# Kernel tuning notes

Hardware: AMD Instinct MI355X
Metric: run time of the kernel (lower is better)

## Reference

```python
import jax, jax.numpy as jnp
import numpy as np

B, T, F, H, L = 16384, 24, 7, 8, 4
DENSE = [T * H, 1024, 2048, 4]


def setup_inputs() -> dict:
    key = jax.random.key(0)
    d = {"x": jax.random.normal(jax.random.fold_in(key, 0), (B, T, F), jnp.float32)}
    k = 1
    s = 1.0 / np.sqrt(H)  # torch LSTM init bound
    for l in range(L):
        in_dim = F if l == 0 else H
        for name, shape in [("Wih", (4 * H, in_dim)), ("Whh", (4 * H, H)), ("bih", (4 * H,)), ("bhh", (4 * H,))]:
            d[f"{name}{l}"] = jax.random.uniform(jax.random.fold_in(key, k), shape, jnp.float32, -s, s)
            k += 1
    for i in range(1, len(DENSE)):
        si = 1.0 / np.sqrt(DENSE[i - 1])
        d[f"Wd{i}"] = jax.random.uniform(jax.random.fold_in(key, k), (DENSE[i], DENSE[i - 1]), jnp.float32, -si, si)
        k += 1
        d[f"bd{i}"] = jax.random.uniform(jax.random.fold_in(key, k), (DENSE[i],), jnp.float32, -si, si)
        k += 1
    return d


def _lstm_layer(xs, Wih, Whh, b):
    # xs: [T, B, in] -> ys: [T, B, H]; torch gate order i,f,g,o
    Hn = Whh.shape[1]
    h0 = jnp.zeros((xs.shape[1], Hn), xs.dtype)

    def step(carry, xt):
        h, c = carry
        z = xt @ Wih.T + h @ Whh.T + b  # [B, 4H]
        i, f, g, o = jnp.split(z, 4, axis=-1)
        c = jax.nn.sigmoid(f) * c + jax.nn.sigmoid(i) * jnp.tanh(g)
        h = jax.nn.sigmoid(o) * jnp.tanh(c)
        return (h, c), h

    (_, _), ys = jax.lax.scan(step, (h0, h0), xs)
    return ys


def _forward(x, lstm_params, dense_params):
    xs = jnp.transpose(x, (1, 0, 2))  # [T, B, F]
    for (Wih, Whh, bih, bhh) in lstm_params:
        xs = _lstm_layer(xs, Wih, Whh, bih + bhh)
    out = jnp.transpose(xs, (1, 0, 2)).reshape(x.shape[0], T * H)  # [B, 192]
    (W1, b1), (W2, b2), (W3, b3) = dense_params
    out = jax.nn.relu(out @ W1.T + b1)
    out = jax.nn.relu(out @ W2.T + b2)
    return out @ W3.T + b3  # [B, num_classes]


def reference(x, Wih0, Whh0, bih0, bhh0, Wih1, Whh1, bih1, bhh1, Wih2, Whh2, bih2, bhh2, Wih3, Whh3, bih3, bhh3, Wd1, bd1, Wd2, bd2, Wd3, bd3):
    lstm_params = [(Wih0, Whh0, bih0, bhh0), (Wih1, Whh1, bih1, bhh1), (Wih2, Whh2, bih2, bhh2), (Wih3, Whh3, bih3, bhh3)]
    dense_params = [(Wd1, bd1), (Wd2, bd2), (Wd3, bd3)]
    return _forward(x, lstm_params, dense_params)
```

## Files before the change

### kernel.cpp

```cpp
#include <hip/hip_runtime.h>
#include <hip/hip_bf16.h>

typedef __attribute__((ext_vector_type(4))) float f32x4;
typedef __attribute__((ext_vector_type(16))) float f32x16;
typedef __attribute__((ext_vector_type(2))) float f32x2;
typedef __attribute__((ext_vector_type(8))) short bf16x8;

__device__ __forceinline__ ushort f2bf(float f) {
    union { float f; uint u; } v; v.f = f;
    uint u = v.u;
    return (ushort)((u + 0x7fffu + ((u >> 16) & 1u)) >> 16);
}
__device__ __forceinline__ float sigm(float x) {
    return __builtin_amdgcn_rcpf(1.0f + __builtin_amdgcn_exp2f(x * -1.442695040888963f));
}
__device__ __forceinline__ float tanh_(float x) {
    return 2.0f * __builtin_amdgcn_rcpf(1.0f + __builtin_amdgcn_exp2f(x * -2.885390081777927f)) - 1.0f;
}

typedef const __attribute__((address_space(1))) unsigned int ga_u32;
typedef __attribute__((address_space(3))) unsigned int lds_u32;
__device__ __forceinline__ void g2l16(const void* g, void* l) {
    __builtin_amdgcn_global_load_lds((ga_u32*)(unsigned long long)g,
                                     (lds_u32*)(unsigned int)(unsigned long long)l,
                                     16, 0, 0);
}

struct LstmW {
    const float* wih[4];
    const float* whh[4];
    const float* bih[4];
    const float* bhh[4];
};

__device__ __forceinline__ void gates8p(const f32x2 w01[8], const f32x2 w23[8],
                                        const float xv8[8], f32x2& a01, f32x2& a23) {
#pragma unroll
    for (int k = 0; k < 8; ++k) {
        f32x2 xv = {xv8[k], xv8[k]};
        a01 += w01[k] * xv;
        a23 += w23[k] * xv;
    }
}
__device__ __forceinline__ void cellup(f32x2 a01, f32x2 a23, float& h, float& c) {
    c = sigm(a01.y) * c + sigm(a01.x) * tanh_(a23.x);
    h = sigm(a23.y) * tanh_(c);
}
__device__ __forceinline__ void ld8(const float* p, float v[8]) {
    float4 a = *(const float4*)p;
    float4 b = *(const float4*)(p + 4);
    v[0] = a.x; v[1] = a.y; v[2] = a.z; v[3] = a.w;
    v[4] = b.x; v[5] = b.y; v[6] = b.z; v[7] = b.w;
}

__global__ __launch_bounds__(256) void pre_kernel(const float* __restrict__ x, LstmW p,
                                                  ushort* __restrict__ Y,
                                                  const float* __restrict__ W1,
                                                  const float* __restrict__ W2,
                                                  ushort* __restrict__ W1b,
                                                  ushort* __restrict__ W2b,
                                                  const float* __restrict__ b3,
                                                  float* __restrict__ out) {
    __shared__ float xs[32 * 168];
    __shared__ float hb[32 * 200];

    const int tid = threadIdx.x;
    if (blockIdx.x >= 512) {
        const int tg = (blockIdx.x - 512) * 256 + tid;
        if (tg < 16384) {
            float4 bv = {b3[0], b3[1], b3[2], b3[3]};
            ((float4*)out)[tg] = bv;
        }
#pragma unroll
        for (int s = 0; s < 4; ++s) {
            int i = tg + s * 143360;
            const float4* src; ushort4* dst; int off;
            if (i < 49152) { src = (const float4*)W1; dst = (ushort4*)W1b; off = i; }
            else { src = (const float4*)W2; dst = (ushort4*)W2b; off = i - 49152; }
            float4 v = src[off];
            ushort4 r; r.x = f2bf(v.x); r.y = f2bf(v.y); r.z = f2bf(v.z); r.w = f2bf(v.w);
            dst[off] = r;
        }
        return;
    }

    const int e0 = blockIdx.x * 32;
    {
        const float4* s = (const float4*)(x + (size_t)e0 * 168);
        float4* d = (float4*)xs;
        for (int i = tid; i < 1344; i += 256) d[i] = s[i];
    }
    __syncthreads();

    const int el = tid >> 3, j = tid & 7;
    float* hr = hb + el * 200;
    const float* xr = xs + el * 168;

    f32x2 wx01[8], wx23[8], wh01[8], wh23[8], b01, b23;

    {
        const float* Wih = p.wih[0];
        const float* Whh = p.whh[0];
#pragma unroll
        for (int k = 0; k < 7; ++k) {
            wx01[k] = {Wih[(0 + j) * 7 + k], Wih[(8 + j) * 7 + k]};
            wx23[k] = {Wih[(16 + j) * 7 + k], Wih[(24 + j) * 7 + k]};
        }
#pragma unroll
        for (int k = 0; k < 8; ++k) {
            wh01[k] = {Whh[(0 + j) * 8 + k], Whh[(8 + j) * 8 + k]};
            wh23[k] = {Whh[(16 + j) * 8 + k], Whh[(24 + j) * 8 + k]};
        }
        b01 = {p.bih[0][j] + p.bhh[0][j], p.bih[0][8 + j] + p.bhh[0][8 + j]};
        b23 = {p.bih[0][16 + j] + p.bhh[0][16 + j], p.bih[0][24 + j] + p.bhh[0][24 + j]};

        float h = 0.f, c = 0.f;
        {
            f32x2 a01 = b01, a23 = b23;
#pragma unroll
            for (int k = 0; k < 7; ++k) {
                f32x2 xv = {xr[k], xr[k]};
                a01 += wx01[k] * xv; a23 += wx23[k] * xv;
            }
            cellup(a01, a23, h, c);
            hr[j] = h;
        }
        for (int t = 1; t < 24; ++t) {
            f32x2 a01 = b01, a23 = b23;
#pragma unroll
            for (int k = 0; k < 7; ++k) {
                f32x2 xv = {xr[t * 7 + k], xr[t * 7 + k]};
                a01 += wx01[k] * xv; a23 += wx23[k] * xv;
            }
            float hp[8]; ld8(&hr[(t - 1) * 8], hp);
            gates8p(wh01, wh23, hp, a01, a23);
            cellup(a01, a23, h, c);
            hr[t * 8 + j] = h;
        }
    }

#pragma unroll
    for (int l = 1; l < 4; ++l) {
        const float* Wih = p.wih[l];
        const float* Whh = p.whh[l];
#pragma unroll
        for (int k = 0; k < 8; ++k) {
            wx01[k] = {Wih[(0 + j) * 8 + k], Wih[(8 + j) * 8 + k]};
            wx23[k] = {Wih[(16 + j) * 8 + k], Wih[(24 + j) * 8 + k]};
            wh01[k] = {Whh[(0 + j) * 8 + k], Whh[(8 + j) * 8 + k]};
            wh23[k] = {Whh[(16 + j) * 8 + k], Whh[(24 + j) * 8 + k]};
        }
        b01 = {p.bih[l][j] + p.bhh[l][j], p.bih[l][8 + j] + p.bhh[l][8 + j]};
        b23 = {p.bih[l][16 + j] + p.bhh[l][16 + j], p.bih[l][24 + j] + p.bhh[l][24 + j]};

        float h = 0.f, c = 0.f;
        {
            float xin[8]; ld8(&hr[0], xin);
            f32x2 a01 = b01, a23 = b23;
            gates8p(wx01, wx23, xin, a01, a23);
            cellup(a01, a23, h, c);
            hr[j] = h;
            if (l == 3) Y[((size_t)(e0 + el) * 24) * 8 + j] = f2bf(h);
        }
        for (int t = 1; t < 24; ++t) {
            float xin[8]; ld8(&hr[t * 8], xin);
            float hp[8];  ld8(&hr[(t - 1) * 8], hp);
            f32x2 a01 = b01, a23 = b23;
            gates8p(wx01, wx23, xin, a01, a23);
            gates8p(wh01, wh23, hp, a01, a23);
            cellup(a01, a23, h, c);
            hr[t * 8 + j] = h;
            if (l == 3) Y[((size_t)(e0 + el) * 24 + t) * 8 + j] = f2bf(h);
        }
    }
}

template <int KDIM, bool FUSE3>
__device__ __forceinline__ void gemm_body(const ushort* __restrict__ A,
                                          const ushort* __restrict__ W,
                                          const float* __restrict__ bias,
                                          ushort* __restrict__ Hout,
                                          const float* __restrict__ W3,
                                          float* __restrict__ outf, int N) {
    constexpr int SMEMN = FUSE3 ? 16896 : 16384;
    __shared__ alignas(16) ushort smem[SMEMN];
    __shared__ alignas(16) float w3s[FUSE3 ? 528 : 1];
    ushort* As = smem;
    ushort* Ws = smem + 8192;

    const int tid = threadIdx.x;
    const int m0 = blockIdx.x * 128;
    const int n0 = blockIdx.y * 128;
    const int lane = tid & 63;
    const int wv = tid >> 6;
    const int wm = (wv & 1) * 64;
    const int wn = (wv >> 1) * 64;
    const int l31 = lane & 31;
    const int kh = lane >> 5;

    if (FUSE3) {
        for (int i = tid; i < 512; i += 256)
            w3s[(i >> 7) * 132 + (i & 127)] = W3[(size_t)(i >> 7) * 2048 + n0 + (i & 127)];
    }

    const int lrow = lane >> 3;
    const int lchunk = (lane & 7) ^ lrow;
    const ushort* Ag = A + (size_t)(m0 + wv * 32 + lrow) * KDIM + lchunk * 8;
    const ushort* Wg = W + (size_t)(n0 + wv * 32 + lrow) * KDIM + lchunk * 8;
    ushort* Ald = As + wv * 2048;
    ushort* Wld = Ws + wv * 2048;

    const int r7 = l31 & 7;
    const int arow0 = (wm + l31) * 64;
    const int brow0 = (wn + l31) * 64;

    f32x16 acc[2][2];
#pragma unroll
    for (int mi = 0; mi < 2; ++mi)
#pragma unroll
        for (int ni = 0; ni < 2; ++ni)
#pragma unroll
            for (int r = 0; r < 16; ++r) acc[mi][ni][r] = 0.f;

    for (int k0 = 0; k0 < KDIM; k0 += 64) {
#pragma unroll
        for (int c = 0; c < 4; ++c)
            g2l16(Ag + (size_t)c * 8 * KDIM + k0, Ald + c * 512);
#pragma unroll
        for (int c = 0; c < 4; ++c)
            g2l16(Wg + (size_t)c * 8 * KDIM + k0, Wld + c * 512);
        __syncthreads();

#pragma unroll
        for (int ks = 0; ks < 4; ++ks) {
            const int ck = ((ks * 2 + kh) ^ r7) * 8;
            bf16x8 afr[2], bfr[2];
#pragma unroll
            for (int mi = 0; mi < 2; ++mi)
                afr[mi] = *(const bf16x8*)&As[arow0 + mi * 2048 + ck];
#pragma unroll
            for (int ni = 0; ni < 2; ++ni)
                bfr[ni] = *(const bf16x8*)&Ws[brow0 + ni * 2048 + ck];
#pragma unroll
            for (int mi = 0; mi < 2; ++mi)
#pragma unroll
                for (int ni = 0; ni < 2; ++ni)
                    acc[mi][ni] = __builtin_amdgcn_mfma_f32_32x32x16_bf16(afr[mi], bfr[ni],
                                                                         acc[mi][ni], 0, 0, 0);
        }
        __syncthreads();
    }

    if (!FUSE3) {
#pragma unroll
        for (int ni = 0; ni < 2; ++ni) {
            const int col = n0 + wn + ni * 32 + l31;
            const float b = bias[col];
#pragma unroll
            for (int mi = 0; mi < 2; ++mi)
#pragma unroll
                for (int r = 0; r < 16; ++r) {
                    const int row = m0 + wm + mi * 32 + (r & 3) + 8 * (r >> 2) + 4 * kh;
                    Hout[(size_t)row * N + col] = f2bf(fmaxf(acc[mi][ni][r] + b, 0.f));
                }
        }
    } else {
        float* Cs = (float*)smem;
        const int drow = tid >> 2;
        const int dn = tid & 3;
#pragma unroll
        for (int pass = 0; pass < 2; ++pass) {
            if ((wv & 1) == pass) {
#pragma unroll
                for (int ni = 0; ni < 2; ++ni) {
                    const int cl = wn + ni * 32 + l31;
                    const float b = bias[n0 + cl];
#pragma unroll
                    for (int mi = 0; mi < 2; ++mi)
#pragma unroll
                        for (int r = 0; r < 16; ++r) {
                            const int rl = mi * 32 + (r & 3) + 8 * (r >> 2) + 4 * kh;
                            Cs[rl * 132 + cl] = fmaxf(acc[mi][ni][r] + b, 0.f);
                        }
                }
            }
            __syncthreads();
            const float* crow = &Cs[drow * 132];
            const float* wrow = &w3s[dn * 132];
            float p = 0.f;
#pragma unroll
            for (int ch = 0; ch < 32; ++ch) {
                f32x4 cv = *(const f32x4*)(crow + ch * 4);
                f32x4 wv4 = *(const f32x4*)(wrow + ch * 4);
                p += cv[0] * wv4[0] + cv[1] * wv4[1] + cv[2] * wv4[2] + cv[3] * wv4[3];
            }
            atomicAdd(&outf[(size_t)(m0 + pass * 64 + drow) * 4 + dn], p);
            __syncthreads();
        }
    }
}

__global__ __launch_bounds__(256, 4) void gemm1_kernel(const ushort* __restrict__ A,
                                                       const ushort* __restrict__ W,
                                                       const float* __restrict__ bias,
                                                       ushort* __restrict__ Hout, int N) {
    gemm_body<192, false>(A, W, bias, Hout, nullptr, nullptr, N);
}
__global__ __launch_bounds__(256, 4) void gemm2_kernel(const ushort* __restrict__ A,
                                                       const ushort* __restrict__ W,
                                                       const float* __restrict__ bias,
                                                       const float* __restrict__ W3,
                                                       float* __restrict__ outf) {
    gemm_body<1024, true>(A, W, bias, nullptr, W3, outf, 2048);
}

extern "C" void kernel_launch(void* const* d_in, const int* in_sizes, int n_in,
                              void* d_out, int out_size, void* d_ws, size_t ws_size,
                              hipStream_t stream) {
    const float* x = (const float*)d_in[0];
    LstmW w;
    for (int l = 0; l < 4; ++l) {
        w.wih[l] = (const float*)d_in[1 + 4 * l];
        w.whh[l] = (const float*)d_in[2 + 4 * l];
        w.bih[l] = (const float*)d_in[3 + 4 * l];
        w.bhh[l] = (const float*)d_in[4 + 4 * l];
    }
    const float* Wd1 = (const float*)d_in[17];
    const float* bd1 = (const float*)d_in[18];
    const float* Wd2 = (const float*)d_in[19];
    const float* bd2 = (const float*)d_in[20];
    const float* Wd3 = (const float*)d_in[21];
    const float* bd3 = (const float*)d_in[22];
    float* out = (float*)d_out;

    ushort* Y   = (ushort*)d_ws;
    ushort* H1  = (ushort*)((char*)d_ws + 6291456);
    ushort* W1b = (ushort*)((char*)d_ws + 39845888);
    ushort* W2b = (ushort*)((char*)d_ws + 40239104);

    pre_kernel<<<1072, 256, 0, stream>>>(x, w, Y, Wd1, Wd2, W1b, W2b, bd3, out);
    gemm1_kernel<<<dim3(128, 8), 256, 0, stream>>>(Y, W1b, bd1, H1, 1024);
    gemm2_kernel<<<dim3(128, 16), 256, 0, stream>>>(H1, W2b, bd2, Wd3, out);
}
```

Baseline: 223.2 us.

## Rewrite second dense GEMM as 256x256-tile, 8-wave ping-pong pipelined kernel

Replaces the 128x128 gemm2 kernel with a 256x256 tile kernel using 512 threads, 16x16x32 MFMA, double-buffered LDS filled by direct global-to-LDS loads, and staggered barriers with s_setprio so loads overlap MFMA work. It also remaps block indices for L2 locality and keeps the fused third dense layer through LDS and atomics, now with 256-wide column slabs. The aim is more operand reuse per tile and better hiding of memory latency in the dominant GEMM. The cost is a large 128KB+ LDS footprint and one block per CU, which leaves only 512 blocks and a complex, fragile sync schedule.

```diff
diff --git a/kernel.cpp b/kernel.cpp
--- a/kernel.cpp
+++ b/kernel.cpp
@@ -175,16 +175,12 @@
     }
 }
 
-template <int KDIM, bool FUSE3>
+template <int KDIM>
 __device__ __forceinline__ void gemm_body(const ushort* __restrict__ A,
                                           const ushort* __restrict__ W,
                                           const float* __restrict__ bias,
-                                          ushort* __restrict__ Hout,
-                                          const float* __restrict__ W3,
-                                          float* __restrict__ outf, int N) {
-    constexpr int SMEMN = FUSE3 ? 16896 : 16384;
-    __shared__ alignas(16) ushort smem[SMEMN];
-    __shared__ alignas(16) float w3s[FUSE3 ? 528 : 1];
+                                          ushort* __restrict__ Hout, int N) {
+    __shared__ alignas(16) ushort smem[16384];
     ushort* As = smem;
     ushort* Ws = smem + 8192;
 
@@ -198,11 +194,6 @@
     const int l31 = lane & 31;
     const int kh = lane >> 5;
 
-    if (FUSE3) {
-        for (int i = tid; i < 512; i += 256)
-            w3s[(i >> 7) * 132 + (i & 127)] = W3[(size_t)(i >> 7) * 2048 + n0 + (i & 127)];
-    }
-
     const int lrow = lane >> 3;
     const int lchunk = (lane & 7) ^ lrow;
     const ushort* Ag = A + (size_t)(m0 + wv * 32 + lrow) * KDIM + lchunk * 8;
@@ -251,52 +242,17 @@
         __syncthreads();
     }
 
-    if (!FUSE3) {
-#pragma unroll
-        for (int ni = 0; ni < 2; ++ni) {
-            const int col = n0 + wn + ni * 32 + l31;
-            const float b = bias[col];
-#pragma unroll
-            for (int mi = 0; mi < 2; ++mi)
-#pragma unroll
-                for (int r = 0; r < 16; ++r) {
-                    const int row = m0 + wm + mi * 32 + (r & 3) + 8 * (r >> 2) + 4 * kh;
-                    Hout[(size_t)row * N + col] = f2bf(fmaxf(acc[mi][ni][r] + b, 0.f));
-                }
-        }
-    } else {
-        float* Cs = (float*)smem;
-        const int drow = tid >> 2;
-        const int dn = tid & 3;
-#pragma unroll
-        for (int pass = 0; pass < 2; ++pass) {
-            if ((wv & 1) == pass) {
-#pragma unroll
-                for (int ni = 0; ni < 2; ++ni) {
-                    const int cl = wn + ni * 32 + l31;
-                    const float b = bias[n0 + cl];
-#pragma unroll
-                    for (int mi = 0; mi < 2; ++mi)
-#pragma unroll
-                        for (int r = 0; r < 16; ++r) {
-                            const int rl = mi * 32 + (r & 3) + 8 * (r >> 2) + 4 * kh;
-                            Cs[rl * 132 + cl] = fmaxf(acc[mi][ni][r] + b, 0.f);
-                        }
-                }
+#pragma unroll
+    for (int ni = 0; ni < 2; ++ni) {
+        const int col = n0 + wn + ni * 32 + l31;
+        const float b = bias[col];
+#pragma unroll
+        for (int mi = 0; mi < 2; ++mi)
+#pragma unroll
+            for (int r = 0; r < 16; ++r) {
+                const int row = m0 + wm + mi * 32 + (r & 3) + 8 * (r >> 2) + 4 * kh;
+                Hout[(size_t)row * N + col] = f2bf(fmaxf(acc[mi][ni][r] + b, 0.f));
             }
-            __syncthreads();
-            const float* crow = &Cs[drow * 132];
-            const float* wrow = &w3s[dn * 132];
-            float p = 0.f;
-#pragma unroll
-            for (int ch = 0; ch < 32; ++ch) {
-                f32x4 cv = *(const f32x4*)(crow + ch * 4);
-                f32x4 wv4 = *(const f32x4*)(wrow + ch * 4);
-                p += cv[0] * wv4[0] + cv[1] * wv4[1] + cv[2] * wv4[2] + cv[3] * wv4[3];
-            }
-            atomicAdd(&outf[(size_t)(m0 + pass * 64 + drow) * 4 + dn], p);
-            __syncthreads();
-        }
     }
 }
 
@@ -304,14 +260,216 @@
                                                        const ushort* __restrict__ W,
                                                        const float* __restrict__ bias,
                                                        ushort* __restrict__ Hout, int N) {
-    gemm_body<192, false>(A, W, bias, Hout, nullptr, nullptr, N);
-}
-__global__ __launch_bounds__(256, 4) void gemm2_kernel(const ushort* __restrict__ A,
-                                                       const ushort* __restrict__ W,
-                                                       const float* __restrict__ bias,
-                                                       const float* __restrict__ W3,
-                                                       float* __restrict__ outf) {
-    gemm_body<1024, true>(A, W, bias, nullptr, W3, outf, 2048);
+    gemm_body<192>(A, W, bias, Hout, N);
+}
+
+__device__ __forceinline__ void ld_ah(const ushort* base, int off, bf16x8 fr[8],
+                                      int pc0, int pc1) {
+#pragma unroll
+    for (int mi = 0; mi < 4; ++mi) {
+        const ushort* p = base + off + mi * 1024;
+        fr[mi * 2 + 0] = *(const bf16x8*)(p + pc0);
+        fr[mi * 2 + 1] = *(const bf16x8*)(p + pc1);
+    }
+}
+__device__ __forceinline__ void ld_bh(const ushort* base, int off, bf16x8 fr[4],
+                                      int pc0, int pc1) {
+#pragma unroll
+    for (int ni = 0; ni < 2; ++ni) {
+        const ushort* p = base + off + ni * 1024;
+        fr[ni * 2 + 0] = *(const bf16x8*)(p + pc0);
+        fr[ni * 2 + 1] = *(const bf16x8*)(p + pc1);
+    }
+}
+template <int QA, int QB>
+__device__ __forceinline__ void mma_quad(f32x4 acc[8][4], const bf16x8 afr[8],
+                                         const bf16x8 bfr[4]) {
+#pragma unroll
+    for (int ks = 0; ks < 2; ++ks)
+#pragma unroll
+        for (int mi = 0; mi < 4; ++mi)
+#pragma unroll
+            for (int ni = 0; ni < 2; ++ni)
+                acc[QA * 4 + mi][QB * 2 + ni] = __builtin_amdgcn_mfma_f32_16x16x32_bf16(
+                    afr[mi * 2 + ks], bfr[ni * 2 + ks], acc[QA * 4 + mi][QB * 2 + ni],
+                    0, 0, 0);
+}
+
+#define SBAR() __builtin_amdgcn_s_barrier()
+
+__global__ __launch_bounds__(512) void gemm2_kernel(const ushort* __restrict__ A,
+                                                    const ushort* __restrict__ W,
+                                                    const float* __restrict__ bias,
+                                                    const float* __restrict__ W3,
+                                                    float* __restrict__ outf) {
+    __shared__ alignas(16) ushort smem[65536];
+    __shared__ alignas(16) float w3s[1040];
+
+    const int tid = threadIdx.x;
+    const int wg = ((int)blockIdx.x & 7) * 64 + ((int)blockIdx.x >> 3);
+    const int m0 = (wg >> 3) << 8;
+    const int n0 = (wg & 7) << 8;
+
+    const int lane = tid & 63;
+    const int wv = tid >> 6;
+
+    const int lrow = tid >> 3;
+    const int lc8 = ((tid & 7) ^ (lrow & 7)) << 3;
+    const ushort* Ag = A + (size_t)(m0 + lrow) * 1024 + lc8;
+    const ushort* Bg = W + (size_t)(n0 + lrow) * 1024 + lc8;
+    ushort* const sA0 = smem;
+    ushort* const sB0 = smem + 16384;
+    ushort* const sA1 = smem + 32768;
+    ushort* const sB1 = smem + 49152;
+    const int srow64 = (wv << 3) * 64;
+
+    const int l15 = lane & 15, kq = lane >> 4, r7 = l15 & 7;
+    const int pc0 = (kq ^ r7) << 3;
+    const int pc1 = ((4 + kq) ^ r7) << 3;
+    const int wM = wv >> 2, wN = wv & 3;
+    const int aOff = (wM * 128 + l15) * 64;
+    const int bOff = (wN * 64 + l15) * 64;
+
+    auto stA = [&](int buf, int h, int kt) {
+        ushort* b = buf ? sA1 : sA0;
+#pragma unroll
+        for (int c = 0; c < 2; ++c)
+            g2l16(Ag + (size_t)(h * 128 + c * 64) * 1024 + kt * 64,
+                  b + (h * 128 + c * 64) * 64 + srow64);
+    };
+    auto stB = [&](int buf, int h, int kt) {
+        ushort* b = buf ? sB1 : sB0;
+#pragma unroll
+        for (int c = 0; c < 2; ++c)
+            g2l16(Bg + (size_t)(h * 128 + c * 64) * 1024 + kt * 64,
+                  b + (h * 128 + c * 64) * 64 + srow64);
+    };
+
+    f32x4 acc[8][4];
+#pragma unroll
+    for (int i = 0; i < 8; ++i)
+#pragma unroll
+        for (int j = 0; j < 4; ++j)
+#pragma unroll
+            for (int r = 0; r < 4; ++r) acc[i][j][r] = 0.f;
+
+#pragma unroll
+    for (int i = 0; i < 2; ++i) {
+        int idx = tid + i * 512;
+        w3s[(idx >> 8) * 260 + (idx & 255)] = W3[(size_t)(idx >> 8) * 2048 + n0 + (idx & 255)];
+    }
+    float bias4[4];
+#pragma unroll
+    for (int ni = 0; ni < 4; ++ni) bias4[ni] = bias[n0 + wN * 64 + ni * 16 + l15];
+
+    stA(0, 0, 0); stB(0, 0, 0); stB(0, 1, 0); stA(0, 1, 0);
+    stB(1, 0, 1); stB(1, 1, 1);
+    asm volatile("s_waitcnt vmcnt(0)" ::: "memory");
+    SBAR();
+
+    bf16x8 afr[8], b0r[4], b1r[4];
+#pragma unroll 1
+    for (int it = 0; it < 8; ++it) {
+        const int k1 = 2 * it + 1, k2 = 2 * it + 2, k3 = 2 * it + 3;
+        const bool nl = (it < 7);
+        ld_ah(sA0, aOff, afr, pc0, pc1);
+        ld_bh(sB0, bOff, b0r, pc0, pc1);
+        stA(1, 0, k1);
+        SBAR();
+        __builtin_amdgcn_s_setprio(1);
+        mma_quad<0, 0>(acc, afr, b0r);
+        __builtin_amdgcn_s_setprio(0);
+        SBAR();
+        ld_bh(sB0, bOff + 2048, b1r, pc0, pc1);
+        stA(1, 1, k1);
+        SBAR();
+        __builtin_amdgcn_s_setprio(1);
+        mma_quad<0, 1>(acc, afr, b1r);
+        __builtin_amdgcn_s_setprio(0);
+        SBAR();
+        ld_ah(sA0, aOff + 4096, afr, pc0, pc1);
+        if (nl) stB(0, 0, k2);
+        SBAR();
+        __builtin_amdgcn_s_setprio(1);
+        mma_quad<1, 1>(acc, afr, b1r);
+        __builtin_amdgcn_s_setprio(0);
+        SBAR();
+        if (nl) stB(0, 1, k2);
+        SBAR();
+        __builtin_amdgcn_s_setprio(1);
+        mma_quad<1, 0>(acc, afr, b0r);
+        __builtin_amdgcn_s_setprio(0);
+        if (nl) { asm volatile("s_waitcnt vmcnt(4)" ::: "memory"); }
+        else    { asm volatile("s_waitcnt vmcnt(0)" ::: "memory"); }
+        SBAR();
+        ld_ah(sA1, aOff + 4096, afr, pc0, pc1);
+        ld_bh(sB1, bOff, b0r, pc0, pc1);
+        if (nl) stA(0, 0, k2);
+        SBAR();
+        __builtin_amdgcn_s_setprio(1);
+        mma_quad<1, 0>(acc, afr, b0r);
+        __builtin_amdgcn_s_setprio(0);
+        SBAR();
+        ld_bh(sB1, bOff + 2048, b1r, pc0, pc1);
+        if (nl) stA(0, 1, k2);
+        SBAR();
+        __builtin_amdgcn_s_setprio(1);
+        mma_quad<1, 1>(acc, afr, b1r);
+        __builtin_amdgcn_s_setprio(0);
+        SBAR();
+        ld_ah(sA1, aOff, afr, pc0, pc1);
+        if (nl) stB(1, 0, k3);
+        SBAR();
+        __builtin_amdgcn_s_setprio(1);
+        mma_quad<0, 1>(acc, afr, b1r);
+        __builtin_amdgcn_s_setprio(0);
+        SBAR();
+        if (nl) stB(1, 1, k3);
+        SBAR();
+        __builtin_amdgcn_s_setprio(1);
+        mma_quad<0, 0>(acc, afr, b0r);
+        __builtin_amdgcn_s_setprio(0);
+        if (nl) { asm volatile("s_waitcnt vmcnt(4)" ::: "memory"); }
+        SBAR();
+    }
+
+    float* Cs = (float*)smem;
+    const int drow = tid >> 3;
+    const int cls = (tid & 7) >> 1;
+    const int hf = tid & 1;
+    const float* wrow = &w3s[cls * 260 + hf * 128];
+    __syncthreads();
+#pragma unroll
+    for (int s = 0; s < 4; ++s) {
+        if (wM == (s >> 1)) {
+            const int mb = (s & 1) * 4;
+#pragma unroll
+            for (int mi = 0; mi < 4; ++mi)
+#pragma unroll
+                for (int ni = 0; ni < 4; ++ni) {
+                    f32x4 v = acc[mb + mi][ni];
+                    const int cbase = (mi * 16 + kq * 4) * 260 + wN * 64 + ni * 16 + l15;
+#pragma unroll
+                    for (int r = 0; r < 4; ++r)
+                        Cs[cbase + r * 260] = fmaxf(v[r] + bias4[ni], 0.f);
+                }
+        }
+        __syncthreads();
+        {
+            const float* crow = &Cs[drow * 260 + hf * 128];
+            float p = 0.f;
+#pragma unroll
+            for (int ch = 0; ch < 64; ++ch) {
+                f32x2 cv = *(const f32x2*)(crow + ch * 2);
+                f32x2 wv2 = *(const f32x2*)(wrow + ch * 2);
+                p += cv.x * wv2.x + cv.y * wv2.y;
+            }
+            p += __shfl_xor(p, 1);
+            if (hf == 0)
+                atomicAdd(&outf[(size_t)(m0 + s * 64 + drow) * 4 + cls], p);
+        }
+        __syncthreads();
+    }
 }
 
 extern "C" void kernel_launch(void* const* d_in, const int* in_sizes, int n_in,
@@ -340,5 +498,5 @@
 
     pre_kernel<<<1072, 256, 0, stream>>>(x, w, Y, Wd1, Wd2, W1b, W2b, bd3, out);
     gemm1_kernel<<<dim3(128, 8), 256, 0, stream>>>(Y, W1b, bd1, H1, 1024);
-    gemm2_kernel<<<dim3(128, 16), 256, 0, stream>>>(H1, W2b, bd2, Wd3, out);
-}
+    gemm2_kernel<<<512, 512, 0, stream>>>(H1, W2b, bd2, Wd3, out);
+}
```

After: 229.5 us. +2.8%, slower.
